# Performance work log

Hardware: AMD Instinct MI355X
Metric: run time of the kernel (lower is better)

Reference implementation:

```python
import jax, jax.numpy as jnp
import numpy as np

M = 0.5
S = 64.0
LS_EPS = 0.0
COS_M = float(np.cos(M))
SIN_M = float(np.sin(M))
THRESHOLD = float(np.cos(np.pi - M))
MM = float(np.sin(np.pi - M) * M)
N_CLASSES = 100000


def setup_inputs() -> dict:
    key = jax.random.key(0)
    k1, k2, k3 = jax.random.split(key, 3)
    embeddings = jax.random.normal(k1, (1024, 512), dtype=jnp.float32)
    kernel = jax.random.normal(k2, (512, N_CLASSES), dtype=jnp.float32) * 0.01
    t = jnp.zeros((1,), dtype=jnp.float32)
    label = jax.random.randint(k3, (1024,), 0, N_CLASSES, dtype=jnp.int64)
    return {"embeddings": embeddings, "kernel": kernel, "t": t, "label": label}


def reference(embeddings, kernel, t, label):
    # l2-normalize embeddings over feature axis, kernel over input axis
    emb = embeddings / jnp.linalg.norm(embeddings, axis=1, keepdims=True)
    kn = kernel / jnp.linalg.norm(kernel, axis=0, keepdims=True)
    cos_theta = jnp.clip(emb @ kn, -1.0, 1.0)  # [N, C]
    n = embeddings.shape[0]
    rows = jnp.arange(n)
    target_logit = cos_theta[rows, label][:, None]  # [N, 1]
    sin_theta = jnp.sqrt(1.0 - target_logit ** 2)
    cos_theta_m = target_logit * COS_M - sin_theta * SIN_M  # [N, 1]
    mask = cos_theta > cos_theta_m  # hard examples (broadcast per row)
    final_target_logit = jnp.where(target_logit > THRESHOLD,
                                   cos_theta_m, target_logit - MM)
    # running-mean buffer update (no-grad in original)
    t_new = jax.lax.stop_gradient(target_logit.mean() * 0.01 + 0.99 * t[0])
    cos_theta = jnp.where(mask, cos_theta * (t_new + cos_theta), cos_theta)
    cos_theta = cos_theta.at[rows, label].set(final_target_logit[:, 0])
    if LS_EPS > 0:
        cos_theta = (1 - LS_EPS) * cos_theta + LS_EPS / N_CLASSES
    return cos_theta * S
```

## Files before the change

kernel.cpp:

```cpp
#include <hip/hip_runtime.h>

typedef unsigned short u16;
typedef unsigned int u32;
typedef __attribute__((ext_vector_type(8))) short bf16x8;
typedef __attribute__((ext_vector_type(4))) float f32x4;

#define KDIM   512
#define NROWS  1024
#define NCLS   100000
#define CPAD   100096
#define NSTRIP 782
#define NMT    8
#define NWG    (NSTRIP*NMT)

#define COS_M_C   0.8775825618903728f
#define SIN_M_C   0.4794255386042030f
#define THRESH_C  (-0.8775825618903728f)
#define MM_C      0.2397127693021015f
#define S_C       64.0f

__device__ __forceinline__ u16 f2bf(float f) {
    u32 x = __float_as_uint(f);
    x += 0x7fffu + ((x >> 16) & 1u);
    return (u16)(x >> 16);
}
__device__ __forceinline__ float bf2f(u16 u) {
    return __uint_as_float(((u32)u) << 16);
}
__device__ __forceinline__ u32 pack2(float a, float b) {
    return (u32)f2bf(a) | ((u32)f2bf(b) << 16);
}

__device__ __forceinline__ int imgoff(int r, int q) {
    return (r >> 1) * 64 + ((((r & 1) << 2) + q + (r >> 1)) & 7) * 8;
}

__device__ __forceinline__ void gld16(const void* g, void* l) {
    __builtin_amdgcn_global_load_lds(
        (const __attribute__((address_space(1))) void*)g,
        (__attribute__((address_space(3))) void*)l, 16, 0, 0);
}

__global__ __launch_bounds__(64)
void norm_emb_k(const float* __restrict__ emb, float* __restrict__ Af,
                u16* __restrict__ Aw) {
    const int i = blockIdx.x, l = threadIdx.x;
    const float* e = emb + i * KDIM;
    float4 v0 = *(const float4*)(e + l * 8);
    float4 v1 = *(const float4*)(e + l * 8 + 4);
    float s = v0.x*v0.x + v0.y*v0.y + v0.z*v0.z + v0.w*v0.w
            + v1.x*v1.x + v1.y*v1.y + v1.z*v1.z + v1.w*v1.w;
    #pragma unroll
    for (int o = 1; o < 64; o <<= 1) s += __shfl_xor(s, o);
    float inv = rsqrtf(s);
    float4 n0 = make_float4(v0.x*inv, v0.y*inv, v0.z*inv, v0.w*inv);
    float4 n1 = make_float4(v1.x*inv, v1.y*inv, v1.z*inv, v1.w*inv);
    *(float4*)(Af + i*KDIM + l*8)     = n0;
    *(float4*)(Af + i*KDIM + l*8 + 4) = n1;
    const int mt = i >> 7, row = i & 127;
    uint4 w;
    w.x = pack2(n0.x, n0.y);
    w.y = pack2(n0.z, n0.w);
    w.z = pack2(n1.x, n1.y);
    w.w = pack2(n1.z, n1.w);
    *(uint4*)(Aw + mt*65536 + (l>>2)*4096 + imgoff(row, l & 3)) = w;
}

__global__ __launch_bounds__(128)
void transpose_norm_k(const float* __restrict__ Kg, u16* __restrict__ Bn,
                      float* __restrict__ kinv) {
    __shared__ float Ls[32 * 132];
    const int t  = threadIdx.x;
    const int jb = blockIdx.x * 128;
    const int j  = jb + t;
    u16* bstrip = Bn + (size_t)blockIdx.x * 65536;
    float acc = 0.f;
    for (int kc = 0; kc < 16; ++kc) {
        #pragma unroll
        for (int it = 0; it < 8; ++it) {
            int fid  = it * 128 + t;
            int r    = fid >> 5;
            int c4   = (fid & 31) * 4;
            int gcol = jb + c4;
            float4 v;
            if (gcol + 3 < NCLS) {
                v = *(const float4*)(Kg + (kc*32 + r) * NCLS + gcol);
            } else {
                v.x = (gcol + 0 < NCLS) ? Kg[(kc*32 + r)*NCLS + gcol + 0] : 0.f;
                v.y = (gcol + 1 < NCLS) ? Kg[(kc*32 + r)*NCLS + gcol + 1] : 0.f;
                v.z = (gcol + 2 < NCLS) ? Kg[(kc*32 + r)*NCLS + gcol + 2] : 0.f;
                v.w = (gcol + 3 < NCLS) ? Kg[(kc*32 + r)*NCLS + gcol + 3] : 0.f;
            }
            *(float4*)(Ls + r * 132 + c4) = v;
        }
        __syncthreads();
        #pragma unroll
        for (int q = 0; q < 4; ++q) {
            u16 u[8];
            #pragma unroll
            for (int e = 0; e < 8; ++e) {
                float v = Ls[(q*8 + e) * 132 + t];
                acc += v * v;
                u[e] = f2bf(v);
            }
            uint4 w;
            w.x = (u32)u[0] | ((u32)u[1] << 16);
            w.y = (u32)u[2] | ((u32)u[3] << 16);
            w.z = (u32)u[4] | ((u32)u[5] << 16);
            w.w = (u32)u[6] | ((u32)u[7] << 16);
            *(uint4*)(bstrip + kc*4096 + imgoff(t, q)) = w;
        }
        __syncthreads();
    }
    kinv[j] = rsqrtf(fmaxf(acc, 1e-30f));
}

__global__ __launch_bounds__(64)
void target_k(const float* __restrict__ Af, const u16* __restrict__ Bn,
              const float* __restrict__ kinv, const int* __restrict__ label,
              float* __restrict__ tgt, float* __restrict__ ctm,
              float* __restrict__ fin) {
    const int i = blockIdx.x, l = threadIdx.x;
    const int lab = label[i];
    float4 a0 = *(const float4*)(Af + i * KDIM + l * 8);
    float4 a1 = *(const float4*)(Af + i * KDIM + l * 8 + 4);
    uint4 bv = *(const uint4*)(Bn + (size_t)(lab >> 7) * 65536
               + (l >> 2) * 4096 + imgoff(lab & 127, l & 3));
    float d = a0.x * bf2f((u16)(bv.x & 0xffff)) + a0.y * bf2f((u16)(bv.x >> 16))
            + a0.z * bf2f((u16)(bv.y & 0xffff)) + a0.w * bf2f((u16)(bv.y >> 16))
            + a1.x * bf2f((u16)(bv.z & 0xffff)) + a1.y * bf2f((u16)(bv.z >> 16))
            + a1.z * bf2f((u16)(bv.w & 0xffff)) + a1.w * bf2f((u16)(bv.w >> 16));
    #pragma unroll
    for (int o = 1; o < 64; o <<= 1) d += __shfl_xor(d, o);
    if (l == 0) {
        float c = d * kinv[lab];
        c = fminf(fmaxf(c, -1.f), 1.f);
        tgt[i] = c;
        float sn = sqrtf(fmaxf(1.f - c*c, 0.f));
        float cm = c * COS_M_C - sn * SIN_M_C;
        ctm[i] = cm;
        fin[i] = (c > THRESH_C) ? cm : (c - MM_C);
    }
}

__global__ __launch_bounds__(256)
void tnew_k(const float* __restrict__ tgt, const float* __restrict__ tin,
            float* __restrict__ tnw) {
    __shared__ float red[256];
    const int t = threadIdx.x;
    float s = tgt[t] + tgt[t + 256] + tgt[t + 512] + tgt[t + 768];
    red[t] = s;
    __syncthreads();
    for (int o = 128; o > 0; o >>= 1) {
        if (t < o) red[t] += red[t + o];
        __syncthreads();
    }
    if (t == 0) tnw[0] = red[0] * (0.01f / 1024.f) + 0.99f * tin[0];
}

__global__ __launch_bounds__(256, 4)
void gemm_k(const u16* __restrict__ A, const u16* __restrict__ B,
            const float* __restrict__ kinv, const float* __restrict__ ctm,
            const float* __restrict__ fin, const int* __restrict__ label,
            const float* __restrict__ tnwp, float* __restrict__ out) {
    __shared__ __align__(16) u16 As[2][4096];
    __shared__ __align__(16) u16 Bs[2][4096];
    const int tid  = threadIdx.x;
    const int wave = tid >> 6, lane = tid & 63;

    const int L  = blockIdx.x;
    const int w  = (L & 7) * NSTRIP + (L >> 3);
    const int mt = w & 7;
    const int cs = w >> 3;
    const int m0 = mt * 128;
    const int j0 = cs * 128;
    const int wr = (wave >> 1) * 64;
    const int wc = (wave & 1) * 64;

    f32x4 acc[4][4] = {};

    const u16* gA = A + mt * 65536 + tid * 8;
    const u16* gB = B + (size_t)cs * 65536 + tid * 8;
    const int  ld = tid * 8;

    const int rowA = wr + (lane & 15);
    const int colB = wc + (lane & 15);
    const int qh   = lane >> 4;
    const int aBase = imgoff(rowA, qh);
    const int bBase = imgoff(colB, qh);

#define STAGE(b, kt) do {                                        \
    gld16(gA + (kt)*4096,        &As[b][ld]);                    \
    gld16(gA + (kt)*4096 + 2048, &As[b][ld + 2048]);             \
    gld16(gB + (kt)*4096,        &Bs[b][ld]);                    \
    gld16(gB + (kt)*4096 + 2048, &Bs[b][ld + 2048]);             \
} while (0)

    STAGE(0, 0);
    #pragma unroll 2
    for (int kt = 0; kt < 16; ++kt) {
        const int cur = kt & 1;
        if (kt < 15) {
            STAGE(cur ^ 1, kt + 1);
            asm volatile("s_waitcnt vmcnt(4)" ::: "memory");
        } else {
            asm volatile("s_waitcnt vmcnt(0)" ::: "memory");
        }
        __builtin_amdgcn_s_barrier();

        bf16x8 af[4], bfr[4];
        #pragma unroll
        for (int m = 0; m < 4; ++m)
            af[m] = *(const bf16x8*)(As[cur] + aBase + m * 512);
        #pragma unroll
        for (int n = 0; n < 4; ++n)
            bfr[n] = *(const bf16x8*)(Bs[cur] + bBase + n * 512);
        asm volatile("s_waitcnt lgkmcnt(0)" ::: "memory");
        __builtin_amdgcn_sched_barrier(0);
        __builtin_amdgcn_s_barrier();

        #pragma unroll
        for (int m = 0; m < 4; ++m)
            #pragma unroll
            for (int n = 0; n < 4; ++n)
                acc[m][n] = __builtin_amdgcn_mfma_f32_16x16x32_bf16(
                                af[m], bfr[n], acc[m][n], 0, 0, 0);
    }
#undef STAGE

    const float tnew = *tnwp;
    const int colbase = j0 + wc + (lane & 15);
    float kv[4];
    int cols[4];
    #pragma unroll
    for (int n = 0; n < 4; ++n) {
        cols[n] = colbase + n * 16;
        kv[n] = kinv[cols[n]];
    }
    #pragma unroll
    for (int m = 0; m < 4; ++m) {
        const int rb = m0 + wr + m * 16 + (lane >> 4) * 4;
        #pragma unroll
        for (int r = 0; r < 4; ++r) {
            const int row = rb + r;
            const int lab = label[row];
            const float ct = ctm[row];
            const float fv = fin[row];
            float* orow = out + (size_t)row * NCLS;
            #pragma unroll
            for (int n = 0; n < 4; ++n) {
                float c = acc[m][n][r] * kv[n];
                c = fminf(fmaxf(c, -1.f), 1.f);
                float v = (c > ct) ? c * (tnew + c) : c;
                v = (cols[n] == lab) ? fv : v;
                if (cols[n] < NCLS)
                    orow[cols[n]] = v * S_C;
            }
        }
    }
}

extern "C" void kernel_launch(void* const* d_in, const int* in_sizes, int n_in,
                              void* d_out, int out_size, void* d_ws, size_t ws_size,
                              hipStream_t stream) {
    const float* emb = (const float*)d_in[0];
    const float* Kg  = (const float*)d_in[1];
    const float* tin = (const float*)d_in[2];
    const int*   lab = (const int*)d_in[3];
    float* out = (float*)d_out;

    char* w = (char*)d_ws;
    u16*   Bn   = (u16*)w;
    u16*   Aw   = (u16*)(w + 102498304);
    float* Af   = (float*)(w + 103546880);
    float* kinv = (float*)(w + 105644032);
    float* tgt  = (float*)(w + 106044416);
    float* ctmv = (float*)(w + 106048512);
    float* finv = (float*)(w + 106052608);
    float* tnw  = (float*)(w + 106056704);

    norm_emb_k<<<NROWS, 64, 0, stream>>>(emb, Af, Aw);
    transpose_norm_k<<<NSTRIP, 128, 0, stream>>>(Kg, Bn, kinv);
    target_k<<<NROWS, 64, 0, stream>>>(Af, Bn, kinv, lab, tgt, ctmv, finv);
    tnew_k<<<1, 256, 0, stream>>>(tgt, tin, tnw);
    gemm_k<<<NWG, 256, 0, stream>>>(
        Aw, Bn, kinv, ctmv, finv, lab, tnw, out);
}
```

Before: 370.5 us.

## Load GEMM fragments directly from global into registers, dropping LDS staging

```diff
diff --git a/kernel.cpp b/kernel.cpp
--- a/kernel.cpp
+++ b/kernel.cpp
@@ -33,12 +33,6 @@
 
 __device__ __forceinline__ int imgoff(int r, int q) {
     return (r >> 1) * 64 + ((((r & 1) << 2) + q + (r >> 1)) & 7) * 8;
-}
-
-__device__ __forceinline__ void gld16(const void* g, void* l) {
-    __builtin_amdgcn_global_load_lds(
-        (const __attribute__((address_space(1))) void*)g,
-        (__attribute__((address_space(3))) void*)l, 16, 0, 0);
 }
 
 __global__ __launch_bounds__(64)
@@ -158,13 +152,11 @@
     if (t == 0) tnw[0] = red[0] * (0.01f / 1024.f) + 0.99f * tin[0];
 }
 
-__global__ __launch_bounds__(256, 4)
+__global__ __launch_bounds__(256)
 void gemm_k(const u16* __restrict__ A, const u16* __restrict__ B,
             const float* __restrict__ kinv, const float* __restrict__ ctm,
             const float* __restrict__ fin, const int* __restrict__ label,
             const float* __restrict__ tnwp, float* __restrict__ out) {
-    __shared__ __align__(16) u16 As[2][4096];
-    __shared__ __align__(16) u16 Bs[2][4096];
     const int tid  = threadIdx.x;
     const int wave = tid >> 6, lane = tid & 63;
 
@@ -179,54 +171,40 @@
 
     f32x4 acc[4][4] = {};
 
-    const u16* gA = A + mt * 65536 + tid * 8;
-    const u16* gB = B + (size_t)cs * 65536 + tid * 8;
-    const int  ld = tid * 8;
-
-    const int rowA = wr + (lane & 15);
-    const int colB = wc + (lane & 15);
-    const int qh   = lane >> 4;
-    const int aBase = imgoff(rowA, qh);
-    const int bBase = imgoff(colB, qh);
-
-#define STAGE(b, kt) do {                                        \
-    gld16(gA + (kt)*4096,        &As[b][ld]);                    \
-    gld16(gA + (kt)*4096 + 2048, &As[b][ld + 2048]);             \
-    gld16(gB + (kt)*4096,        &Bs[b][ld]);                    \
-    gld16(gB + (kt)*4096 + 2048, &Bs[b][ld + 2048]);             \
+    const int lr = lane & 15, q = lane >> 4;
+    const u16* aP = A + mt * 65536 + imgoff(wr + lr, q);
+    const u16* bP = B + (size_t)cs * 65536 + imgoff(wc + lr, q);
+
+    bf16x8 a0[4], b0[4], a1[4], b1[4];
+
+#define LOADF(AS, BS, kt) do {                                       \
+    const u16* ap_ = aP + (kt) * 4096;                               \
+    const u16* bp_ = bP + (kt) * 4096;                               \
+    _Pragma("unroll")                                                \
+    for (int m = 0; m < 4; ++m) AS[m] = *(const bf16x8*)(ap_ + m * 512); \
+    _Pragma("unroll")                                                \
+    for (int n = 0; n < 4; ++n) BS[n] = *(const bf16x8*)(bp_ + n * 512); \
 } while (0)
 
-    STAGE(0, 0);
-    #pragma unroll 2
-    for (int kt = 0; kt < 16; ++kt) {
-        const int cur = kt & 1;
-        if (kt < 15) {
-            STAGE(cur ^ 1, kt + 1);
-            asm volatile("s_waitcnt vmcnt(4)" ::: "memory");
-        } else {
-            asm volatile("s_waitcnt vmcnt(0)" ::: "memory");
-        }
-        __builtin_amdgcn_s_barrier();
-
-        bf16x8 af[4], bfr[4];
-        #pragma unroll
-        for (int m = 0; m < 4; ++m)
-            af[m] = *(const bf16x8*)(As[cur] + aBase + m * 512);
-        #pragma unroll
-        for (int n = 0; n < 4; ++n)
-            bfr[n] = *(const bf16x8*)(Bs[cur] + bBase + n * 512);
-        asm volatile("s_waitcnt lgkmcnt(0)" ::: "memory");
-        __builtin_amdgcn_sched_barrier(0);
-        __builtin_amdgcn_s_barrier();
-
-        #pragma unroll
-        for (int m = 0; m < 4; ++m)
-            #pragma unroll
-            for (int n = 0; n < 4; ++n)
-                acc[m][n] = __builtin_amdgcn_mfma_f32_16x16x32_bf16(
-                                af[m], bfr[n], acc[m][n], 0, 0, 0);
-    }
-#undef STAGE
+#define MFMA16(AS, BS) do {                                          \
+    _Pragma("unroll")                                                \
+    for (int m = 0; m < 4; ++m)                                      \
+        _Pragma("unroll")                                            \
+        for (int n = 0; n < 4; ++n)                                  \
+            acc[m][n] = __builtin_amdgcn_mfma_f32_16x16x32_bf16(     \
+                            AS[m], BS[n], acc[m][n], 0, 0, 0);       \
+} while (0)
+
+    LOADF(a0, b0, 0);
+    #pragma unroll
+    for (int kt = 0; kt < 16; kt += 2) {
+        if (kt + 1 < 16) LOADF(a1, b1, kt + 1);
+        MFMA16(a0, b0);
+        if (kt + 2 < 16) LOADF(a0, b0, kt + 2);
+        if (kt + 1 < 16) MFMA16(a1, b1);
+    }
+#undef LOADF
+#undef MFMA16
 
     const float tnew = *tnwp;
     const int colbase = j0 + wc + (lane & 15);
```

New measurement: 403.2 us. +8.8%, slower.

## Stage GEMM epilogue through LDS for coalesced float4 output stores

Applied to the files above, without the earlier changes.

```diff
diff --git a/kernel.cpp b/kernel.cpp
--- a/kernel.cpp
+++ b/kernel.cpp
@@ -181,19 +181,16 @@
 
     const u16* gA = A + mt * 65536 + tid * 8;
     const u16* gB = B + (size_t)cs * 65536 + tid * 8;
-    const int  ld = tid * 8;
-
-    const int rowA = wr + (lane & 15);
-    const int colB = wc + (lane & 15);
-    const int qh   = lane >> 4;
-    const int aBase = imgoff(rowA, qh);
-    const int bBase = imgoff(colB, qh);
+
+    const int lr = lane & 15, q = lane >> 4;
+    const int aBase = imgoff(wr + lr, q);
+    const int bBase = imgoff(wc + lr, q);
 
 #define STAGE(b, kt) do {                                        \
-    gld16(gA + (kt)*4096,        &As[b][ld]);                    \
-    gld16(gA + (kt)*4096 + 2048, &As[b][ld + 2048]);             \
-    gld16(gB + (kt)*4096,        &Bs[b][ld]);                    \
-    gld16(gB + (kt)*4096 + 2048, &Bs[b][ld + 2048]);             \
+    gld16(gA + (kt)*4096,        &As[b][tid*8]);                 \
+    gld16(gA + (kt)*4096 + 2048, &As[b][tid*8 + 2048]);          \
+    gld16(gB + (kt)*4096,        &Bs[b][tid*8]);                 \
+    gld16(gB + (kt)*4096 + 2048, &Bs[b][tid*8 + 2048]);          \
 } while (0)
 
     STAGE(0, 0);
@@ -229,34 +226,52 @@
 #undef STAGE
 
     const float tnew = *tnwp;
-    const int colbase = j0 + wc + (lane & 15);
-    float kv[4];
-    int cols[4];
-    #pragma unroll
-    for (int n = 0; n < 4; ++n) {
-        cols[n] = colbase + n * 16;
-        kv[n] = kinv[cols[n]];
-    }
-    #pragma unroll
+    float* slab = (float*)As;
+    const int srd  = tid >> 3;
+    const int cseg = (tid & 7) * 16;
+    #pragma unroll 1
     for (int m = 0; m < 4; ++m) {
-        const int rb = m0 + wr + m * 16 + (lane >> 4) * 4;
-        #pragma unroll
-        for (int r = 0; r < 4; ++r) {
-            const int row = rb + r;
-            const int lab = label[row];
-            const float ct = ctm[row];
-            const float fv = fin[row];
-            float* orow = out + (size_t)row * NCLS;
+        __builtin_amdgcn_s_barrier();
+        const int swr = (wr >> 6) * 16 + q * 4;
+        #pragma unroll
+        for (int n = 0; n < 4; ++n) {
+            const int col = wc + n * 16 + lr;
             #pragma unroll
-            for (int n = 0; n < 4; ++n) {
-                float c = acc[m][n][r] * kv[n];
-                c = fminf(fmaxf(c, -1.f), 1.f);
-                float v = (c > ct) ? c * (tnew + c) : c;
-                v = (cols[n] == lab) ? fv : v;
-                if (cols[n] < NCLS)
-                    orow[cols[n]] = v * S_C;
+            for (int r = 0; r < 4; ++r)
+                slab[(swr + r) * 132 + col] = acc[m][n][r];
+        }
+        asm volatile("s_waitcnt lgkmcnt(0)" ::: "memory");
+        __builtin_amdgcn_s_barrier();
+        const int grow = m0 + (srd >> 4) * 64 + m * 16 + (srd & 15);
+        const int cb   = j0 + cseg;
+        const float ct  = ctm[grow];
+        const float fv  = fin[grow];
+        const int   lab = label[grow];
+        float* op = out + (size_t)grow * NCLS + cb;
+        #pragma unroll
+        for (int v4 = 0; v4 < 4; ++v4) {
+            const int c0 = cb + v4 * 4;
+            float4 kv4 = *(const float4*)(kinv + c0);
+            const float* kvp = (const float*)&kv4;
+            float o[4];
+            #pragma unroll
+            for (int c = 0; c < 4; ++c) {
+                float x = slab[srd * 132 + cseg + v4 * 4 + c] * kvp[c];
+                x = fminf(fmaxf(x, -1.f), 1.f);
+                float v = (x > ct) ? x * (tnew + x) : x;
+                v = (c0 + c == lab) ? fv : v;
+                o[c] = v * S_C;
             }
-        }
+            if (c0 + 3 < NCLS) {
+                *(float4*)(op + v4 * 4) = make_float4(o[0], o[1], o[2], o[3]);
+            } else {
+                #pragma unroll
+                for (int c = 0; c < 4; ++c)
+                    if (c0 + c < NCLS) op[v4 * 4 + c] = o[c];
+            }
+        }
+        asm volatile("s_waitcnt lgkmcnt(0)" ::: "memory");
+        __builtin_amdgcn_sched_barrier(0);
     }
 }
 
```

After: 586.4 us. 1.58x slower.
